# Optimization experiments

Measured on AMD Instinct MI355X. Metric: run time of the kernel, lower is better.

Reference implementation:

```python
import jax, jax.numpy as jnp
import numpy as np

EMBED_DIM = 1024
NUM_HEADS = 16
HEAD_DIM = EMBED_DIM // NUM_HEADS  # 64
B, H_P, W_P = 4, 48, 48
N = H_P * W_P  # 2304


def setup_inputs() -> dict:
    key = jax.random.key(0)
    ks = jax.random.split(key, 12)
    s = 1.0 / np.sqrt(EMBED_DIM)
    inp = {
        "query": jax.random.normal(ks[0], (B, N, EMBED_DIM), jnp.float32),
        "key": jax.random.normal(ks[1], (B, N, EMBED_DIM), jnp.float32),
        "value": jax.random.normal(ks[2], (B, N, EMBED_DIM), jnp.float32),
        "Wq": jax.random.normal(ks[3], (EMBED_DIM, EMBED_DIM), jnp.float32) * s,
        "bq": jnp.zeros((EMBED_DIM,), jnp.float32),
        "Wk": jax.random.normal(ks[4], (EMBED_DIM, EMBED_DIM), jnp.float32) * s,
        "bk": jnp.zeros((EMBED_DIM,), jnp.float32),
        "Wv": jax.random.normal(ks[5], (EMBED_DIM, EMBED_DIM), jnp.float32) * s,
        "bv": jnp.zeros((EMBED_DIM,), jnp.float32),
        "Wo": jax.random.normal(ks[6], (EMBED_DIM, EMBED_DIM), jnp.float32) * s,
        "bo": jnp.zeros((EMBED_DIM,), jnp.float32),
        "H_patch": H_P,
        "W_patch": W_P,
    }
    return inp


def _rope_2d_cos_sin(h_idx, w_idx, head_dim):
    # 2D RoPE: first half of head_dim encodes the y axis, second half the x axis.
    half = head_dim // 2          # dims per spatial axis (32)
    inv_freq = 1.0 / (10000.0 ** (jnp.arange(0, half, 2, dtype=jnp.float32) / half))  # [half//2]
    fh = h_idx.astype(jnp.float32)[:, None] * inv_freq[None, :]  # [N, half//2]
    fw = w_idx.astype(jnp.float32)[:, None] * inv_freq[None, :]
    emb_h = jnp.concatenate([fh, fh], axis=-1)  # [N, half]
    emb_w = jnp.concatenate([fw, fw], axis=-1)
    emb = jnp.concatenate([emb_h, emb_w], axis=-1)  # [N, head_dim]
    return jnp.cos(emb), jnp.sin(emb)


def _rotate_half_seg(x):
    # rotate_half within a per-axis segment
    h = x.shape[-1] // 2
    return jnp.concatenate([-x[..., h:], x[..., :h]], axis=-1)


def _apply_rotary_2d(x, cos, sin):
    # x: [B, H, N, head_dim]; cos/sin: [N, head_dim]
    half = x.shape[-1] // 2
    c = cos[None, None]
    s = sin[None, None]
    xh, xw = x[..., :half], x[..., half:]
    ch, cw = c[..., :half], c[..., half:]
    sh, sw = s[..., :half], s[..., half:]
    yh = xh * ch + _rotate_half_seg(xh) * sh
    yw = xw * cw + _rotate_half_seg(xw) * sw
    return jnp.concatenate([yh, yw], axis=-1)


def reference(query, key, value, Wq, bq, Wk, bk, Wv, bv, Wo, bo, H_patch, W_patch):
    Bsz, Nn, D = query.shape
    hd = D // NUM_HEADS

    def split_heads(x):
        return x.reshape(Bsz, Nn, NUM_HEADS, hd).transpose(0, 2, 1, 3)  # [B,H,N,hd]

    q = split_heads(query @ Wq.T + bq)
    k = split_heads(key @ Wk.T + bk)
    v = split_heads(value @ Wv.T + bv)

    ys = jnp.arange(H_patch)
    xs = jnp.arange(W_patch)
    yy, xx = jnp.meshgrid(ys, xs, indexing="ij")
    cos, sin = _rope_2d_cos_sin(yy.reshape(-1), xx.reshape(-1), hd)

    q = _apply_rotary_2d(q, cos, sin)
    k = _apply_rotary_2d(k, cos, sin)

    scale = hd ** (-0.5)
    attn = jnp.einsum("bhnd,bhmd->bhnm", q, k) * scale
    attn = jax.nn.softmax(attn, axis=-1)
    out = jnp.einsum("bhnm,bhmd->bhnd", attn, v)
    out = out.transpose(0, 2, 1, 3).reshape(Bsz, Nn, D)
    return out @ Wo.T + bo
```

## Files before the change

### kernel.cpp

```cpp
#include <hip/hip_runtime.h>
#include <cstdint>
#include <cstddef>


typedef __bf16 bf16x8 __attribute__((ext_vector_type(8)));
typedef __bf16 bf16x4 __attribute__((ext_vector_type(4)));
typedef __fp16 fp16v2 __attribute__((ext_vector_type(2)));
typedef _Float16 f16x4 __attribute__((ext_vector_type(4)));
typedef _Float16 f16x8 __attribute__((ext_vector_type(8)));
typedef float f32x4 __attribute__((ext_vector_type(4)));

constexpr int Bc = 4, Hc = 16, Nc = 2304, Ec = 1024, WPc = 48;
constexpr int BNc = Bc * Nc;

__device__ __forceinline__ f32x4 mfma16(bf16x8 a, bf16x8 b, f32x4 c) {
  return __builtin_amdgcn_mfma_f32_16x16x32_bf16(a, b, c, 0, 0, 0);
}
__device__ __forceinline__ f32x4 mfmah32(f16x8 a, f16x8 b, f32x4 c) {
  return __builtin_amdgcn_mfma_f32_16x16x32_f16(a, b, c, 0, 0, 0);
}

#define GPTR(p) ((const __attribute__((address_space(1))) void*)(p))
#define LPTR(p) ((__attribute__((address_space(3))) void*)(p))

__global__ __launch_bounds__(256) void cvt_bf16(const float* __restrict__ s,
                                                __bf16* __restrict__ d, int n) {
  int i = (blockIdx.x * 256 + threadIdx.x) * 8;
  if (i >= n) return;
  float4 f0 = *(const float4*)(s + i);
  float4 f1 = *(const float4*)(s + i + 4);
  bf16x8 v;
  v[0] = (__bf16)f0.x; v[1] = (__bf16)f0.y; v[2] = (__bf16)f0.z; v[3] = (__bf16)f0.w;
  v[4] = (__bf16)f1.x; v[5] = (__bf16)f1.y; v[6] = (__bf16)f1.z; v[7] = (__bf16)f1.w;
  *(bf16x8*)(d + i) = v;
}

#define GEMM_CORE(APTR, WPTR, KDIM)                                             \
  __shared__ __align__(16) __bf16 As[128 * 32];                                 \
  __shared__ __align__(16) __bf16 Bs[128 * 32];                                 \
  const int t = threadIdx.x;                                                    \
  const int lane = t & 63, wave = t >> 6;                                       \
  const int wm = wave & 1, wn = wave >> 1;                                      \
  const int quad = lane >> 4, l15 = lane & 15;                                  \
  const int rowInC = lane >> 2, colC = (lane & 3) * 8;                          \
  const __bf16* Ab = (APTR) + (size_t)(tm * 128) * (KDIM);                      \
  const __bf16* Wb = (WPTR) + (size_t)(tn * 128) * (KDIM);                      \
  f32x4 zero = {0.f, 0.f, 0.f, 0.f};                                            \
  f32x4 acc[4][4];                                                              \
  for (int i = 0; i < 4; ++i)                                                   \
    for (int j = 0; j < 4; ++j) acc[i][j] = zero;                               \
  for (int kk = 0; kk < (KDIM); kk += 32) {                                     \
    _Pragma("unroll") for (int tch = 0; tch < 2; ++tch) {                       \
      const int ch = wave * 2 + tch;                                            \
      const int row = ch * 16 + rowInC;                                         \
      __builtin_amdgcn_global_load_lds(GPTR(Ab + (size_t)row * (KDIM) + kk + colC), \
                                       LPTR(As + ch * 512), 16, 0, 0);          \
      __builtin_amdgcn_global_load_lds(GPTR(Wb + (size_t)row * (KDIM) + kk + colC), \
                                       LPTR(Bs + ch * 512), 16, 0, 0);          \
    }                                                                           \
    __syncthreads();                                                            \
    bf16x8 af[4], bfg[4];                                                       \
    _Pragma("unroll") for (int i = 0; i < 4; ++i)                               \
        af[i] = *(const bf16x8*)(As + (wm * 64 + i * 16 + l15) * 32 + quad * 8);\
    _Pragma("unroll") for (int j = 0; j < 4; ++j)                               \
        bfg[j] = *(const bf16x8*)(Bs + (wn * 64 + j * 16 + l15) * 32 + quad * 8);\
    _Pragma("unroll") for (int i = 0; i < 4; ++i)                               \
      _Pragma("unroll") for (int j = 0; j < 4; ++j)                             \
        acc[i][j] = mfma16(af[i], bfg[j], acc[i][j]);                           \
    __syncthreads();                                                            \
  }                                                                             \
  const int m0 = tm * 128 + wm * 64;                                            \
  const int nb0 = tn * 128 + wn * 64;

__global__ __launch_bounds__(256) void gemm_qk(const __bf16* __restrict__ qkb,
                                               const __bf16* __restrict__ Wqk,
                                               const float* __restrict__ bq,
                                               const float* __restrict__ bk,
                                               __bf16* __restrict__ Qhp,
                                               __bf16* __restrict__ Khp,
                                               float qscale) {
  const int tn = blockIdx.x & 15;
  const int tm = blockIdx.x >> 4;
  const int proj = tn >> 3;
  const __bf16* Asel = qkb + (size_t)proj * BNc * Ec;
  GEMM_CORE(Asel, Wqk, Ec)

  const int h = (nb0 >> 6) & 15;
  const float scale = proj ? 1.0f : qscale;
  __bf16* O = proj ? Khp : Qhp;
  const float* bb = proj ? bk : bq;
  float bj[4];
#pragma unroll
  for (int j = 0; j < 4; ++j) bj[j] = bb[(nb0 + j * 16 + l15) & 1023];
  const float f = exp2f(-(float)l15 * 0.8304820237218406f);
  const int lo3 = l15 & 7, hi8 = l15 >> 3;
#pragma unroll
  for (int i = 0; i < 4; ++i) {
#pragma unroll
    for (int r = 0; r < 4; ++r) {
      const int m = m0 + i * 16 + quad * 4 + r;
      const int b = m / Nc;
      const int ntok = m - b * Nc;
      const int ph = ntok / WPc, pw = ntok - (ntok / WPc) * WPc;
      float sh, ch, sw, cw;
      __sincosf((float)ph * f, &sh, &ch);
      __sincosf((float)pw * f, &sw, &cw);
      const float x0 = acc[i][0][r] + bj[0];
      const float x1 = acc[i][1][r] + bj[1];
      const float x2 = acc[i][2][r] + bj[2];
      const float x3 = acc[i][3][r] + bj[3];
      int wtok = ntok;
      if (proj) {
        const int t64 = ntok & 63;
        wtok = (ntok & ~63) | (t64 & 35) | ((t64 & 4) << 2) | ((t64 & 24) >> 1);
      }
      __bf16* Op = O + ((size_t)(b * Hc + h) * Nc + wtok) * 64;
      const int n7 = proj ? (wtok & 7) : 0;
      Op[(((0 + hi8) ^ n7) << 3) | lo3] = (__bf16)((x0 * ch - x1 * sh) * scale);
      Op[(((2 + hi8) ^ n7) << 3) | lo3] = (__bf16)((x1 * ch + x0 * sh) * scale);
      Op[(((4 + hi8) ^ n7) << 3) | lo3] = (__bf16)((x2 * cw - x3 * sw) * scale);
      Op[(((6 + hi8) ^ n7) << 3) | lo3] = (__bf16)((x3 * cw + x2 * sw) * scale);
    }
  }
}

__global__ __launch_bounds__(256) void gemm_v(const __bf16* __restrict__ A,
                                              const __bf16* __restrict__ Wv,
                                              const float* __restrict__ bv,
                                              _Float16* __restrict__ Vt) {
  const int tn = blockIdx.x & 7;
  const int tm = blockIdx.x >> 3;
  GEMM_CORE(A, Wv, Ec)

  const int h = nb0 >> 6;
#pragma unroll
  for (int i = 0; i < 4; ++i) {
    const int m = m0 + i * 16 + quad * 4;
    const int b = m / Nc;
    const int ntok = m - b * Nc;
    const int base = (ntok >> 6) * 64 + (((ntok >> 2) & 1) << 2);
    const int c8 = (ntok >> 3) & 7;
#pragma unroll
    for (int j = 0; j < 4; ++j) {
      const int d = j * 16 + l15;
      const float bi = bv[nb0 + j * 16 + l15];
      f16x4 v;
#pragma unroll
      for (int r = 0; r < 4; ++r) v[r] = (_Float16)(acc[i][j][r] + bi);
      const int off = base + ((c8 ^ (l15 & 7)) << 3);
      *(f16x4*)(Vt + ((size_t)(b * Hc + h) * 64 + d) * Nc + off) = v;
    }
  }
}

__global__ __launch_bounds__(256) void gemm_out(const __bf16* __restrict__ A,
                                                const __bf16* __restrict__ Wo,
                                                const float* __restrict__ bo,
                                                float* __restrict__ C) {
  const int tn = blockIdx.x & 7;
  const int tm = blockIdx.x >> 3;
  GEMM_CORE(A, Wo, Ec)

#pragma unroll
  for (int j = 0; j < 4; ++j) {
    const int n = nb0 + j * 16 + l15;
    const float bi = bo[n];
#pragma unroll
    for (int i = 0; i < 4; ++i) {
      const int m = m0 + i * 16 + quad * 4;
#pragma unroll
      for (int r = 0; r < 4; ++r) C[(size_t)(m + r) * Ec + n] = acc[i][j][r] + bi;
    }
  }
}

constexpr int TQ = 128, TK = 64, NT = Nc / TK;

__global__ __launch_bounds__(256) void attn(const __bf16* __restrict__ Qh,
                                            const __bf16* __restrict__ Kg,
                                            const _Float16* __restrict__ Vg,
                                            __bf16* __restrict__ Om) {
  const int bh = blockIdx.x;
  const int t = threadIdx.x, wave = t >> 6, lane = t & 63;
  const int quad = lane >> 4, l15 = lane & 15;

  __shared__ __align__(16) __bf16 Kls[3][TK * 64];
  __shared__ __align__(16) _Float16 Vls[3][TK * 64];

  const int qbase = blockIdx.y * TQ + wave * 32;
  bf16x8 bq[2][2];
#pragma unroll
  for (int s = 0; s < 2; ++s)
#pragma unroll
    for (int ks = 0; ks < 2; ++ks)
      bq[s][ks] = *(const bf16x8*)(Qh + ((size_t)bh * Nc + qbase + s * 16 + l15) * 64 +
                                   ks * 32 + quad * 8);
#pragma unroll
  for (int s = 0; s < 2; ++s)
#pragma unroll
    for (int ks = 0; ks < 2; ++ks) asm volatile("" : "+v"(bq[s][ks]));
  asm volatile("s_waitcnt vmcnt(0)" ::: "memory");

  const __bf16* Kbh = Kg + (size_t)bh * Nc * 64;
  const _Float16* Vbh = Vg + (size_t)bh * 64 * Nc;

  const f32x4 zero = {0.f, 0.f, 0.f, 0.f};
  f32x4 oacc[2][4] = {{zero, zero, zero, zero}, {zero, zero, zero, zero}};
  f32x4 osum[2] = {zero, zero};
  const f16x8 fones8 = {(_Float16)1.f, (_Float16)1.f, (_Float16)1.f, (_Float16)1.f,
                        (_Float16)1.f, (_Float16)1.f, (_Float16)1.f, (_Float16)1.f};

  const int vrow = lane >> 3, vcol = (lane & 7) * 8;

#define STAGE(KT2, BUF2)                                                        \
  {                                                                             \
    _Pragma("unroll") for (int i = 0; i < 2; ++i) {                             \
      const int ch = wave * 2 + i;                                              \
      __builtin_amdgcn_global_load_lds(                                         \
          GPTR(Kbh + (size_t)(KT2) * (TK * 64) + ch * 512 + lane * 8),          \
          LPTR(&Kls[BUF2][ch * 512]), 16, 0, 0);                                \
    }                                                                           \
    _Pragma("unroll") for (int i = 0; i < 2; ++i) {                             \
      const int ch = wave * 2 + i;                                              \
      const int d = ch * 8 + vrow;                                              \
      __builtin_amdgcn_global_load_lds(                                         \
          GPTR(Vbh + (size_t)d * Nc + (size_t)(KT2) * 64 + vcol),               \
          LPTR(&Vls[BUF2][ch * 512]), 16, 0, 0);                                \
    }                                                                           \
  }

#define COMPUTE(BUF)                                                            \
  {                                                                             \
    f32x4 sacc[2][4] = {{zero, zero, zero, zero}, {zero, zero, zero, zero}};    \
    __builtin_amdgcn_s_setprio(1);                                              \
    _Pragma("unroll") for (int ks = 0; ks < 2; ++ks) {                          \
      _Pragma("unroll") for (int ct = 0; ct < 4; ++ct) {                        \
        const bf16x8 ak = *(const bf16x8*)(&Kls[BUF][(ct * 16 + l15) * 64 +     \
            (((ks * 4 + quad) ^ (l15 & 7)) << 3)]);                             \
        sacc[0][ct] = mfma16(ak, bq[0][ks], sacc[0][ct]);                       \
        sacc[1][ct] = mfma16(ak, bq[1][ks], sacc[1][ct]);                       \
      }                                                                         \
    }                                                                           \
    __builtin_amdgcn_s_setprio(0);                                              \
    f16x8 pf[2][2];                                                             \
    _Pragma("unroll") for (int s = 0; s < 2; ++s)                               \
      _Pragma("unroll") for (int c2 = 0; c2 < 2; ++c2) {                        \
        union { fp16v2 h2[4]; f16x8 h8; } u;                                    \
        u.h2[0] = __builtin_amdgcn_cvt_pkrtz(exp2f(sacc[s][2 * c2][0]),         \
                                             exp2f(sacc[s][2 * c2][1]));        \
        u.h2[1] = __builtin_amdgcn_cvt_pkrtz(exp2f(sacc[s][2 * c2][2]),         \
                                             exp2f(sacc[s][2 * c2][3]));        \
        u.h2[2] = __builtin_amdgcn_cvt_pkrtz(exp2f(sacc[s][2 * c2 + 1][0]),     \
                                             exp2f(sacc[s][2 * c2 + 1][1]));    \
        u.h2[3] = __builtin_amdgcn_cvt_pkrtz(exp2f(sacc[s][2 * c2 + 1][2]),     \
                                             exp2f(sacc[s][2 * c2 + 1][3]));    \
        pf[s][c2] = u.h8;                                                       \
      }                                                                         \
    __builtin_amdgcn_s_setprio(1);                                              \
    _Pragma("unroll") for (int c2 = 0; c2 < 2; ++c2) {                          \
      _Pragma("unroll") for (int dt = 0; dt < 4; ++dt) {                        \
        const f16x8 av = *(const f16x8*)(&Vls[BUF][(dt * 16 + l15) * 64 +       \
            (((c2 * 4 + quad) ^ (l15 & 7)) << 3)]);                             \
        oacc[0][dt] = mfmah32(av, pf[0][c2], oacc[0][dt]);                      \
        oacc[1][dt] = mfmah32(av, pf[1][c2], oacc[1][dt]);                      \
      }                                                                         \
      osum[0] = mfmah32(fones8, pf[0][c2], osum[0]);                            \
      osum[1] = mfmah32(fones8, pf[1][c2], osum[1]);                            \
    }                                                                           \
    __builtin_amdgcn_s_setprio(0);                                              \
  }

#define PHASE(KT, BUF, WN, DS)                                                  \
  asm volatile("s_waitcnt vmcnt(" #WN ")" ::: "memory");                        \
  __builtin_amdgcn_s_barrier();                                                 \
  asm volatile("" ::: "memory");                                                \
  if (DS) STAGE((KT) + 2, ((BUF) + 2) % 3)                                      \
  COMPUTE(BUF)

  STAGE(0, 0)
  STAGE(1, 1)

#pragma unroll 1
  for (int kt = 0; kt < NT - 3; kt += 3) {
    PHASE(kt, 0, 4, 1)
    PHASE(kt + 1, 1, 4, 1)
    PHASE(kt + 2, 2, 4, 1)
  }
  PHASE(NT - 3, 0, 4, 1)
  PHASE(NT - 2, 1, 4, 0)
  PHASE(NT - 1, 2, 0, 0)

  const int b = bh >> 4, h = bh & 15;
#pragma unroll
  for (int s = 0; s < 2; ++s) {
    const float rinv = 1.0f / osum[s][0];
    __bf16* Op = Om + ((size_t)b * Nc + qbase + s * 16 + l15) * Ec + h * 64 + quad * 4;
#pragma unroll
    for (int dt = 0; dt < 4; ++dt) {
      bf16x4 o;
#pragma unroll
      for (int r = 0; r < 4; ++r) o[r] = (__bf16)(oacc[s][dt][r] * rinv);
      *(bf16x4*)(Op + dt * 16) = o;
    }
  }
#undef STAGE
#undef COMPUTE
#undef PHASE
}

extern "C" void kernel_launch(void* const* d_in, const int* in_sizes, int n_in,
                              void* d_out, int out_size, void* d_ws, size_t ws_size,
                              hipStream_t stream) {
  const float* q  = (const float*)d_in[0];
  const float* k  = (const float*)d_in[1];
  const float* v  = (const float*)d_in[2];
  const float* Wq = (const float*)d_in[3];
  const float* bq = (const float*)d_in[4];
  const float* Wk = (const float*)d_in[5];
  const float* bk = (const float*)d_in[6];
  const float* Wv = (const float*)d_in[7];
  const float* bv = (const float*)d_in[8];
  const float* Wo = (const float*)d_in[9];
  const float* bo = (const float*)d_in[10];
  float* out = (float*)d_out;

  const size_t EE = (size_t)Ec * Ec;
  const size_t BNE = (size_t)BNc * Ec;

  char* w = (char*)d_ws;
  __bf16* Wqkb = (__bf16*)w; w += 2 * EE * 2;
  __bf16* Wvb  = (__bf16*)w; w += EE * 2;
  __bf16* Wob  = (__bf16*)w; w += EE * 2;
  __bf16* qb   = (__bf16*)w; w += BNE * 2;
  __bf16* kb   = (__bf16*)w; w += BNE * 2;
  __bf16* vb   = (__bf16*)w; w += BNE * 2;
  __bf16* Qhp  = (__bf16*)w; w += BNE * 2;
  __bf16* Khp  = (__bf16*)w; w += BNE * 2;
  _Float16* Vtp = (_Float16*)kb;
  __bf16* Omp = qb;

  const dim3 blk(256);
  const dim3 gCvtW(EE / 8 / 256);
  const dim3 gCvtA(BNE / 8 / 256);
  const dim3 gQK(16 * (BNc / 128));
  const dim3 gG(8 * (BNc / 128));
  const dim3 gAttn(Bc * Hc, Nc / TQ);

  cvt_bf16<<<gCvtW, blk, 0, stream>>>(Wq, Wqkb, (int)EE);
  cvt_bf16<<<gCvtW, blk, 0, stream>>>(Wk, Wqkb + EE, (int)EE);
  cvt_bf16<<<gCvtW, blk, 0, stream>>>(Wv, Wvb, (int)EE);
  cvt_bf16<<<gCvtW, blk, 0, stream>>>(Wo, Wob, (int)EE);
  cvt_bf16<<<gCvtA, blk, 0, stream>>>(q, qb, (int)BNE);
  cvt_bf16<<<gCvtA, blk, 0, stream>>>(k, kb, (int)BNE);
  cvt_bf16<<<gCvtA, blk, 0, stream>>>(v, vb, (int)BNE);

  const float qscale = 0.125f * 1.44269504088896340736f;

  gemm_qk<<<gQK, blk, 0, stream>>>(qb, Wqkb, bq, bk, Qhp, Khp, qscale);
  gemm_v<<<gG, blk, 0, stream>>>(vb, Wvb, bv, Vtp);
  attn<<<gAttn, blk, 0, stream>>>(Qhp, Khp, Vtp, Omp);
  gemm_out<<<gG, blk, 0, stream>>>(Omp, Wob, bo, out);
}
```

Baseline: 490.3 us.

## Double attention query tile to 256 with 512-thread blocks sharing K/V staging

The attention kernel now runs 8 waves per block over a 256-query tile, so each staged K/V tile in LDS serves twice as many queries. Each wave issues one K and one V global-to-LDS load per stage instead of two of each, and the vmcnt waits are adjusted to match. The grid shrinks to 64x9 blocks, which raises K/V reuse but lowers the block count and may hurt occupancy or CU balance. The exp-to-fp16 packing also changes from cvt_pkrtz intrinsics to plain casts, which may alter rounding mode and instruction count.

```diff
diff --git a/kernel.cpp b/kernel.cpp
--- a/kernel.cpp
+++ b/kernel.cpp
@@ -5,7 +5,6 @@
 
 typedef __bf16 bf16x8 __attribute__((ext_vector_type(8)));
 typedef __bf16 bf16x4 __attribute__((ext_vector_type(4)));
-typedef __fp16 fp16v2 __attribute__((ext_vector_type(2)));
 typedef _Float16 f16x4 __attribute__((ext_vector_type(4)));
 typedef _Float16 f16x8 __attribute__((ext_vector_type(8)));
 typedef float f32x4 __attribute__((ext_vector_type(4)));
@@ -174,9 +173,9 @@
   }
 }
 
-constexpr int TQ = 128, TK = 64, NT = Nc / TK;
-
-__global__ __launch_bounds__(256) void attn(const __bf16* __restrict__ Qh,
+constexpr int TQ = 256, TK = 64, NT = Nc / TK;
+
+__global__ __launch_bounds__(512) void attn(const __bf16* __restrict__ Qh,
                                             const __bf16* __restrict__ Kg,
                                             const _Float16* __restrict__ Vg,
                                             __bf16* __restrict__ Om) {
@@ -214,19 +213,13 @@
 
 #define STAGE(KT2, BUF2)                                                        \
   {                                                                             \
-    _Pragma("unroll") for (int i = 0; i < 2; ++i) {                             \
-      const int ch = wave * 2 + i;                                              \
-      __builtin_amdgcn_global_load_lds(                                         \
-          GPTR(Kbh + (size_t)(KT2) * (TK * 64) + ch * 512 + lane * 8),          \
-          LPTR(&Kls[BUF2][ch * 512]), 16, 0, 0);                                \
-    }                                                                           \
-    _Pragma("unroll") for (int i = 0; i < 2; ++i) {                             \
-      const int ch = wave * 2 + i;                                              \
-      const int d = ch * 8 + vrow;                                              \
-      __builtin_amdgcn_global_load_lds(                                         \
-          GPTR(Vbh + (size_t)d * Nc + (size_t)(KT2) * 64 + vcol),               \
-          LPTR(&Vls[BUF2][ch * 512]), 16, 0, 0);                                \
-    }                                                                           \
+    __builtin_amdgcn_global_load_lds(                                           \
+        GPTR(Kbh + (size_t)(KT2) * (TK * 64) + wave * 512 + lane * 8),          \
+        LPTR(&Kls[BUF2][wave * 512]), 16, 0, 0);                                \
+    const int dV = wave * 8 + vrow;                                             \
+    __builtin_amdgcn_global_load_lds(                                           \
+        GPTR(Vbh + (size_t)dV * Nc + (size_t)(KT2) * 64 + vcol),                \
+        LPTR(&Vls[BUF2][wave * 512]), 16, 0, 0);                                \
   }
 
 #define COMPUTE(BUF)                                                            \
@@ -245,16 +238,10 @@
     f16x8 pf[2][2];                                                             \
     _Pragma("unroll") for (int s = 0; s < 2; ++s)                               \
       _Pragma("unroll") for (int c2 = 0; c2 < 2; ++c2) {                        \
-        union { fp16v2 h2[4]; f16x8 h8; } u;                                    \
-        u.h2[0] = __builtin_amdgcn_cvt_pkrtz(exp2f(sacc[s][2 * c2][0]),         \
-                                             exp2f(sacc[s][2 * c2][1]));        \
-        u.h2[1] = __builtin_amdgcn_cvt_pkrtz(exp2f(sacc[s][2 * c2][2]),         \
-                                             exp2f(sacc[s][2 * c2][3]));        \
-        u.h2[2] = __builtin_amdgcn_cvt_pkrtz(exp2f(sacc[s][2 * c2 + 1][0]),     \
-                                             exp2f(sacc[s][2 * c2 + 1][1]));    \
-        u.h2[3] = __builtin_amdgcn_cvt_pkrtz(exp2f(sacc[s][2 * c2 + 1][2]),     \
-                                             exp2f(sacc[s][2 * c2 + 1][3]));    \
-        pf[s][c2] = u.h8;                                                       \
+        _Pragma("unroll") for (int r = 0; r < 4; ++r) {                         \
+          pf[s][c2][r]     = (_Float16)exp2f(sacc[s][2 * c2][r]);               \
+          pf[s][c2][4 + r] = (_Float16)exp2f(sacc[s][2 * c2 + 1][r]);           \
+        }                                                                       \
       }                                                                         \
     __builtin_amdgcn_s_setprio(1);                                              \
     _Pragma("unroll") for (int c2 = 0; c2 < 2; ++c2) {                          \
@@ -282,12 +269,12 @@
 
 #pragma unroll 1
   for (int kt = 0; kt < NT - 3; kt += 3) {
-    PHASE(kt, 0, 4, 1)
-    PHASE(kt + 1, 1, 4, 1)
-    PHASE(kt + 2, 2, 4, 1)
-  }
-  PHASE(NT - 3, 0, 4, 1)
-  PHASE(NT - 2, 1, 4, 0)
+    PHASE(kt, 0, 2, 1)
+    PHASE(kt + 1, 1, 2, 1)
+    PHASE(kt + 2, 2, 2, 1)
+  }
+  PHASE(NT - 3, 0, 2, 1)
+  PHASE(NT - 2, 1, 2, 0)
   PHASE(NT - 1, 2, 0, 0)
 
   const int b = bh >> 4, h = bh & 15;
@@ -340,6 +327,7 @@
   __bf16* Omp = qb;
 
   const dim3 blk(256);
+  const dim3 blkA(512);
   const dim3 gCvtW(EE / 8 / 256);
   const dim3 gCvtA(BNE / 8 / 256);
   const dim3 gQK(16 * (BNc / 128));
@@ -358,6 +346,6 @@
 
   gemm_qk<<<gQK, blk, 0, stream>>>(qb, Wqkb, bq, bk, Qhp, Khp, qscale);
   gemm_v<<<gG, blk, 0, stream>>>(vb, Wvb, bv, Vtp);
-  attn<<<gAttn, blk, 0, stream>>>(Qhp, Khp, Vtp, Omp);
+  attn<<<gAttn, blkA, 0, stream>>>(Qhp, Khp, Vtp, Omp);
   gemm_out<<<gG, blk, 0, stream>>>(Omp, Wob, bo, out);
 }
```

Measured after the change: 508.1 us. 1.04x slower.

## Split K/V staging: triple-buffer K, double-buffer V to cut LDS footprint

Applied to the files above, without the earlier changes.

Splits the attention tile prefetch into separate K and V stages. K keeps a three-deep LDS ring while V drops to two buffers and is fetched only one tile ahead. The loop is unrolled by six to cycle both buffer indices, with adjusted vmcnt waits. This shrinks LDS per block, which could allow more resident blocks, but leaves less time to hide V load latency. It also replaces the packed cvt_pkrtz exp conversion with plain per-element half casts, which may change the rounding mode and the instructions emitted.

```diff
diff --git a/kernel.cpp b/kernel.cpp
--- a/kernel.cpp
+++ b/kernel.cpp
@@ -5,7 +5,6 @@
 
 typedef __bf16 bf16x8 __attribute__((ext_vector_type(8)));
 typedef __bf16 bf16x4 __attribute__((ext_vector_type(4)));
-typedef __fp16 fp16v2 __attribute__((ext_vector_type(2)));
 typedef _Float16 f16x4 __attribute__((ext_vector_type(4)));
 typedef _Float16 f16x8 __attribute__((ext_vector_type(8)));
 typedef float f32x4 __attribute__((ext_vector_type(4)));
@@ -185,7 +184,7 @@
   const int quad = lane >> 4, l15 = lane & 15;
 
   __shared__ __align__(16) __bf16 Kls[3][TK * 64];
-  __shared__ __align__(16) _Float16 Vls[3][TK * 64];
+  __shared__ __align__(16) _Float16 Vls[2][TK * 64];
 
   const int qbase = blockIdx.y * TQ + wave * 32;
   bf16x8 bq[2][2];
@@ -212,7 +211,7 @@
 
   const int vrow = lane >> 3, vcol = (lane & 7) * 8;
 
-#define STAGE(KT2, BUF2)                                                        \
+#define STAGE_K(KT2, BUF2)                                                      \
   {                                                                             \
     _Pragma("unroll") for (int i = 0; i < 2; ++i) {                             \
       const int ch = wave * 2 + i;                                              \
@@ -220,6 +219,9 @@
           GPTR(Kbh + (size_t)(KT2) * (TK * 64) + ch * 512 + lane * 8),          \
           LPTR(&Kls[BUF2][ch * 512]), 16, 0, 0);                                \
     }                                                                           \
+  }
+#define STAGE_V(KT2, BUF2)                                                      \
+  {                                                                             \
     _Pragma("unroll") for (int i = 0; i < 2; ++i) {                             \
       const int ch = wave * 2 + i;                                              \
       const int d = ch * 8 + vrow;                                              \
@@ -229,13 +231,13 @@
     }                                                                           \
   }
 
-#define COMPUTE(BUF)                                                            \
+#define COMPUTE(KB, VB)                                                         \
   {                                                                             \
     f32x4 sacc[2][4] = {{zero, zero, zero, zero}, {zero, zero, zero, zero}};    \
     __builtin_amdgcn_s_setprio(1);                                              \
     _Pragma("unroll") for (int ks = 0; ks < 2; ++ks) {                          \
       _Pragma("unroll") for (int ct = 0; ct < 4; ++ct) {                        \
-        const bf16x8 ak = *(const bf16x8*)(&Kls[BUF][(ct * 16 + l15) * 64 +     \
+        const bf16x8 ak = *(const bf16x8*)(&Kls[KB][(ct * 16 + l15) * 64 +      \
             (((ks * 4 + quad) ^ (l15 & 7)) << 3)]);                             \
         sacc[0][ct] = mfma16(ak, bq[0][ks], sacc[0][ct]);                       \
         sacc[1][ct] = mfma16(ak, bq[1][ks], sacc[1][ct]);                       \
@@ -245,21 +247,15 @@
     f16x8 pf[2][2];                                                             \
     _Pragma("unroll") for (int s = 0; s < 2; ++s)                               \
       _Pragma("unroll") for (int c2 = 0; c2 < 2; ++c2) {                        \
-        union { fp16v2 h2[4]; f16x8 h8; } u;                                    \
-        u.h2[0] = __builtin_amdgcn_cvt_pkrtz(exp2f(sacc[s][2 * c2][0]),         \
-                                             exp2f(sacc[s][2 * c2][1]));        \
-        u.h2[1] = __builtin_amdgcn_cvt_pkrtz(exp2f(sacc[s][2 * c2][2]),         \
-                                             exp2f(sacc[s][2 * c2][3]));        \
-        u.h2[2] = __builtin_amdgcn_cvt_pkrtz(exp2f(sacc[s][2 * c2 + 1][0]),     \
-                                             exp2f(sacc[s][2 * c2 + 1][1]));    \
-        u.h2[3] = __builtin_amdgcn_cvt_pkrtz(exp2f(sacc[s][2 * c2 + 1][2]),     \
-                                             exp2f(sacc[s][2 * c2 + 1][3]));    \
-        pf[s][c2] = u.h8;                                                       \
+        _Pragma("unroll") for (int r = 0; r < 4; ++r) {                         \
+          pf[s][c2][r]     = (_Float16)exp2f(sacc[s][2 * c2][r]);               \
+          pf[s][c2][4 + r] = (_Float16)exp2f(sacc[s][2 * c2 + 1][r]);           \
+        }                                                                       \
       }                                                                         \
     __builtin_amdgcn_s_setprio(1);                                              \
     _Pragma("unroll") for (int c2 = 0; c2 < 2; ++c2) {                          \
       _Pragma("unroll") for (int dt = 0; dt < 4; ++dt) {                        \
-        const f16x8 av = *(const f16x8*)(&Vls[BUF][(dt * 16 + l15) * 64 +       \
+        const f16x8 av = *(const f16x8*)(&Vls[VB][(dt * 16 + l15) * 64 +        \
             (((c2 * 4 + quad) ^ (l15 & 7)) << 3)]);                             \
         oacc[0][dt] = mfmah32(av, pf[0][c2], oacc[0][dt]);                      \
         oacc[1][dt] = mfmah32(av, pf[1][c2], oacc[1][dt]);                      \
@@ -270,25 +266,33 @@
     __builtin_amdgcn_s_setprio(0);                                              \
   }
 
-#define PHASE(KT, BUF, WN, DS)                                                  \
+#define PHASE(KT, KB, VB, VSB, KSB, WN, DV, DK)                                 \
   asm volatile("s_waitcnt vmcnt(" #WN ")" ::: "memory");                        \
   __builtin_amdgcn_s_barrier();                                                 \
   asm volatile("" ::: "memory");                                                \
-  if (DS) STAGE((KT) + 2, ((BUF) + 2) % 3)                                      \
-  COMPUTE(BUF)
-
-  STAGE(0, 0)
-  STAGE(1, 1)
+  if (DV) STAGE_V((KT) + 1, VSB)                                                \
+  if (DK) STAGE_K((KT) + 2, KSB)                                                \
+  COMPUTE(KB, VB)
+
+  STAGE_V(0, 0)
+  STAGE_K(0, 0)
+  STAGE_K(1, 1)
 
 #pragma unroll 1
-  for (int kt = 0; kt < NT - 3; kt += 3) {
-    PHASE(kt, 0, 4, 1)
-    PHASE(kt + 1, 1, 4, 1)
-    PHASE(kt + 2, 2, 4, 1)
-  }
-  PHASE(NT - 3, 0, 4, 1)
-  PHASE(NT - 2, 1, 4, 0)
-  PHASE(NT - 1, 2, 0, 0)
+  for (int kt = 0; kt < NT - 6; kt += 6) {
+    PHASE(kt + 0, 0, 0, 1, 2, 2, 1, 1)
+    PHASE(kt + 1, 1, 1, 0, 0, 2, 1, 1)
+    PHASE(kt + 2, 2, 0, 1, 1, 2, 1, 1)
+    PHASE(kt + 3, 0, 1, 0, 2, 2, 1, 1)
+    PHASE(kt + 4, 1, 0, 1, 0, 2, 1, 1)
+    PHASE(kt + 5, 2, 1, 0, 1, 2, 1, 1)
+  }
+  PHASE(30, 0, 0, 1, 2, 2, 1, 1)
+  PHASE(31, 1, 1, 0, 0, 2, 1, 1)
+  PHASE(32, 2, 0, 1, 1, 2, 1, 1)
+  PHASE(33, 0, 1, 0, 2, 2, 1, 1)
+  PHASE(34, 1, 0, 1, 0, 2, 1, 0)
+  PHASE(35, 2, 1, 0, 0, 0, 0, 0)
 
   const int b = bh >> 4, h = bh & 15;
 #pragma unroll
@@ -303,7 +307,8 @@
       *(bf16x4*)(Op + dt * 16) = o;
     }
   }
-#undef STAGE
+#undef STAGE_K
+#undef STAGE_V
 #undef COMPUTE
 #undef PHASE
 }
```

Result: no change. 484.7 us (-1.1%).
